# Optimization experiments

Measured on AMD Instinct MI355X. Metric: run time of the kernel, lower is better.

## Reference

```python
import jax, jax.numpy as jnp
import numpy as np

N_TARGETS = 4
BATCH_SIZE = 4
B = N_TARGETS * BATCH_SIZE
N_SAMPLES = 1024
LAYERS = [(128, 128), (256, 64), (512, 32)]  # (channels, spatial)
EPS_COS = 1e-10


def setup_inputs() -> dict:
    key = jax.random.key(0)
    inp = {}
    for l, (c, s) in enumerate(LAYERS):
        k1, k2, k3, k4, key = jax.random.split(key, 5)
        n = s * s
        inp[f't{l}'] = jax.random.normal(k1, (N_TARGETS, c, s, s), dtype=jnp.float32)
        inp[f'g{l}'] = jax.random.normal(k2, (B, c, s, s), dtype=jnp.float32)
        inp[f'ix{l}'] = jax.random.randint(k3, (B, N_SAMPLES), 0, n)
        inp[f'iy{l}'] = jax.random.randint(k4, (B, N_SAMPLES), 0, n)
    return inp


def _cos_remd(x, y):
    # x: (b,n,c), y: (b,m,c)
    xn = jnp.linalg.norm(x, axis=2, keepdims=True)            # (b,n,1)
    yn = jnp.linalg.norm(y, axis=2, keepdims=True)            # (b,m,1)
    cross = jnp.einsum('bnc,bmc->bnm', x, y)                  # (b,n,m)
    dist = 1.0 - cross / (xn * yn.transpose(0, 2, 1) + EPS_COS)
    m1 = dist.min(axis=1).mean(axis=1)                        # min over n, mean over m
    m2 = dist.min(axis=2).mean(axis=1)                        # min over m, mean over n
    return jnp.maximum(m1, m2)                                # (b,)


def _moment_loss(x, y):
    mu_x = x.mean(axis=1, keepdims=True)
    mu_y = y.mean(axis=1, keepdims=True)
    mu_diff = jnp.abs(mu_x - mu_y).mean(axis=(1, 2))
    x_c = x - mu_x
    y_c = y - mu_y
    x_cov = jnp.einsum('bnc,bnd->bcd', x_c, x_c) / (x.shape[1] - 1)
    y_cov = jnp.einsum('bmc,bmd->bcd', y_c, y_c) / (y.shape[1] - 1)
    cov_diff = jnp.abs(x_cov - y_cov).mean(axis=(1, 2))
    return mu_diff + cov_diff                                 # (b,)


def _layer_loss(t, g, ix, iy):
    b, c, h, w = g.shape
    y = jnp.tile(t, (BATCH_SIZE, 1, 1, 1)).reshape(b, t.shape[1], -1)  # (b,c,n_y)
    x = g.reshape(b, c, -1)                                            # (b,c,n_x)
    x = jnp.take_along_axis(x, ix[:, None, :], axis=2)                 # (b,c,ns)
    y = jnp.take_along_axis(y, iy[:, None, :], axis=2)                 # (b,c,ns)
    x = x.transpose(0, 2, 1)
    y = y.transpose(0, 2, 1)
    return _cos_remd(x, y) + _moment_loss(x, y)


def reference(t0, g0, t1, g1, t2, g2, ix0, iy0, ix1, iy1, ix2, iy2):
    loss = (_layer_loss(t0, g0, ix0, iy0)
            + _layer_loss(t1, g1, ix1, iy1)
            + _layer_loss(t2, g2, ix2, iy2))
    return loss.reshape(BATCH_SIZE, N_TARGETS).mean(axis=0)   # (n_targets,)
```

## Files before the change

kernel.cpp:

```cpp
#include <hip/hip_runtime.h>
#include <math.h>

#define NT 4
#define BSZ 4
#define BB 16
#define NS 1024
#define CHF 1024
#define NBUF 4
#define MAXL 3

typedef unsigned short u16;
typedef __attribute__((ext_vector_type(8))) short bf16x8;
typedef __attribute__((ext_vector_type(4))) float f32x4;

struct LayerP {
    const float *g, *t;
    const int *ix, *iy;
    u16 *Xt, *Yt, *Xs, *Ys;
    float *xp, *yp;
    float *rxn, *ryn;
    float *sx, *sy;
    unsigned *m1u, *m2u;
    float *cov;
    int C, n, nchunk, ntri, lid;
};
struct Tab {
    LayerP L[MAXL];
    int nl, nb, b0, ysh;
    float* losspart;
};

__device__ __forceinline__ unsigned fenc(float f) {
    unsigned u = __float_as_uint(f);
    return (u & 0x80000000u) ? ~u : (u | 0x80000000u);
}
__device__ __forceinline__ float fdec(unsigned u) {
    unsigned v = (u & 0x80000000u) ? (u & 0x7FFFFFFFu) : ~u;
    return __uint_as_float(v);
}
__device__ __forceinline__ u16 f2bf(float f) {
    unsigned u = __float_as_uint(f);
    unsigned r = u + 0x7FFFu + ((u >> 16) & 1u);
    return (u16)(r >> 16);
}
__device__ __forceinline__ float bf2f(u16 h) {
    return __uint_as_float((unsigned)h << 16);
}

__device__ __forceinline__ void gload16(const float* src, float* dst) {
    __builtin_amdgcn_global_load_lds(
        (const __attribute__((address_space(1))) float*)src,
        (__attribute__((address_space(3))) float*)dst, 16, 0, 0);
}
__device__ __forceinline__ void wait_rem(int rem) {
    if (rem >= 2)      asm volatile("s_waitcnt vmcnt(2)" ::: "memory");
    else if (rem == 1) asm volatile("s_waitcnt vmcnt(1)" ::: "memory");
    else               asm volatile("s_waitcnt vmcnt(0)" ::: "memory");
}

__global__ __launch_bounds__(256) void gather_x(Tab tab)
{
    int x = blockIdx.x, l = 0;
    while (l < MAXL - 1 && x >= tab.L[l].C) { x -= tab.L[l].C; ++l; }
    const LayerP P = tab.L[l];
    int c = x, bl = blockIdx.y, bg = tab.b0 + bl;
    int tid = threadIdx.x;
    int wv = tid >> 6, lane = tid & 63;
    const float* __restrict__ grow = P.g + ((size_t)bg * P.C + c) * P.n;
    const int* __restrict__ ixr = P.ix + bg * NS;
    __shared__ __align__(16) float buf[NBUF][CHF];
    __shared__ float red[4];
    int px[4];
    float xv[4] = {0.f, 0.f, 0.f, 0.f};
    #pragma unroll
    for (int r = 0; r < 4; ++r) px[r] = ixr[tid + r * 256];
    int nch = P.n >> 10;
    int npro = nch < 3 ? nch : 3;
    for (int d = 0; d < npro; ++d)
        gload16(grow + d * CHF + wv * 256 + lane * 4, &buf[d][wv * 256]);
    for (int ch = 0; ch < nch; ++ch) {
        int rem = nch - 1 - ch; if (rem > 2) rem = 2;
        wait_rem(rem);
        __builtin_amdgcn_s_barrier();
        __builtin_amdgcn_sched_barrier(0);
        if (ch + 3 < nch)
            gload16(grow + (ch + 3) * CHF + wv * 256 + lane * 4, &buf[(ch + 3) & 3][wv * 256]);
        int lo = ch * CHF;
        #pragma unroll
        for (int r = 0; r < 4; ++r) {
            int rel = px[r] - lo;
            if ((unsigned)rel < (unsigned)CHF) xv[r] = buf[ch & 3][rel];
        }
    }
    u16* __restrict__ xo = P.Xt + ((size_t)bl * P.C + c) * NS;
    float ax = 0.f;
    #pragma unroll
    for (int r = 0; r < 4; ++r) {
        u16 hb = f2bf(xv[r]);
        xo[tid + r * 256] = hb;
        ax += bf2f(hb);
    }
    for (int o = 32; o > 0; o >>= 1) ax += __shfl_down(ax, o);
    if (lane == 0) red[wv] = ax;
    __syncthreads();
    if (tid == 0) P.sx[bl * P.C + c] = red[0] + red[1] + red[2] + red[3];
}

__global__ __launch_bounds__(256) void gather_y(Tab tab)
{
    int x = blockIdx.x, l = 0;
    while (l < MAXL - 1 && x >= tab.L[l].C) { x -= tab.L[l].C; ++l; }
    const LayerP P = tab.L[l];
    int c = x, grp = blockIdx.y;
    int tid = threadIdx.x;
    int wv = tid >> 6, lane = tid & 63;
    int nk, tgt, bls[4];
    if (tab.ysh == NT) {
        nk = 4; tgt = grp;
        #pragma unroll
        for (int k = 0; k < 4; ++k) bls[k] = grp + NT * k;
    } else {
        nk = 1; bls[0] = grp; tgt = (tab.b0 + grp) % NT;
        bls[1] = bls[2] = bls[3] = 0;
    }
    const float* __restrict__ trow = P.t + ((size_t)tgt * P.C + c) * P.n;
    __shared__ __align__(16) float buf[NBUF][CHF];
    __shared__ float red[4][4];
    int py[4][4];
    float yv[4][4];
    #pragma unroll
    for (int k = 0; k < 4; ++k) {
        if (k < nk) {
            const int* iyr = P.iy + (tab.b0 + bls[k]) * NS;
            #pragma unroll
            for (int r = 0; r < 4; ++r) { py[k][r] = iyr[tid + r * 256]; yv[k][r] = 0.f; }
        }
    }
    int nch = P.n >> 10;
    int npro = nch < 3 ? nch : 3;
    for (int d = 0; d < npro; ++d)
        gload16(trow + d * CHF + wv * 256 + lane * 4, &buf[d][wv * 256]);
    for (int ch = 0; ch < nch; ++ch) {
        int rem = nch - 1 - ch; if (rem > 2) rem = 2;
        wait_rem(rem);
        __builtin_amdgcn_s_barrier();
        __builtin_amdgcn_sched_barrier(0);
        if (ch + 3 < nch)
            gload16(trow + (ch + 3) * CHF + wv * 256 + lane * 4, &buf[(ch + 3) & 3][wv * 256]);
        int lo = ch * CHF;
        #pragma unroll
        for (int k = 0; k < 4; ++k)
            if (k < nk) {
                #pragma unroll
                for (int r = 0; r < 4; ++r) {
                    int rel = py[k][r] - lo;
                    if ((unsigned)rel < (unsigned)CHF) yv[k][r] = buf[ch & 3][rel];
                }
            }
    }
    #pragma unroll
    for (int k = 0; k < 4; ++k) {
        if (k >= nk) break;
        u16* __restrict__ yo = P.Yt + ((size_t)bls[k] * P.C + c) * NS;
        float ay = 0.f;
        #pragma unroll
        for (int r = 0; r < 4; ++r) {
            u16 hb = f2bf(yv[k][r]);
            yo[tid + r * 256] = hb;
            ay += bf2f(hb);
        }
        for (int o = 32; o > 0; o >>= 1) ay += __shfl_down(ay, o);
        if (lane == 0) red[k][wv] = ay;
    }
    __syncthreads();
    if (tid < nk)
        P.sy[bls[tid] * P.C + c] = red[tid][0] + red[tid][1] + red[tid][2] + red[tid][3];
}

__global__ void transpose_k(Tab tab)
{
    int x = blockIdx.x, l = 0;
    while (l < MAXL - 1 && x >= tab.L[l].C / 64) { x -= tab.L[l].C / 64; ++l; }
    const LayerP P = tab.L[l];
    int z = blockIdx.z;
    int bl = z >> 1, which = z & 1;
    const u16* __restrict__ Zt = which ? P.Yt : P.Xt;
    u16* __restrict__ Zs = which ? P.Ys : P.Xs;
    float* __restrict__ zp = which ? P.yp : P.xp;
    int C = P.C;
    int ctile = x;
    int c0 = ctile * 64, s0 = blockIdx.y * 64;
    __shared__ __align__(16) u16 T[64][72];
    int tid = threadIdx.x;
    #pragma unroll
    for (int rep = 0; rep < 2; ++rep) {
        int q = tid + rep * 256;
        int rr = q >> 3, seg = q & 7;
        *(float4*)&T[rr][seg * 8] =
            *(const float4*)&Zt[((size_t)bl * C + c0 + rr) * NS + s0 + seg * 8];
    }
    __syncthreads();
    #pragma unroll
    for (int rep = 0; rep < 2; ++rep) {
        int q = tid + rep * 256;
        int sr = q >> 3, cs = q & 7;
        __align__(16) u16 tmp[8];
        float p = 0.f;
        #pragma unroll
        for (int e = 0; e < 8; ++e) {
            u16 h = T[cs * 8 + e][sr];
            tmp[e] = h;
            float v = bf2f(h);
            p = fmaf(v, v, p);
        }
        *(float4*)&Zs[((size_t)bl * NS + s0 + sr) * C + c0 + cs * 8] = *(float4*)tmp;
        p += __shfl_xor(p, 1);
        p += __shfl_xor(p, 2);
        p += __shfl_xor(p, 4);
        if (cs == 0)
            zp[((size_t)bl * P.nchunk + ctile) * NS + s0 + sr] = p;
    }
}

__global__ void colnorm_reduce(Tab tab)
{
    const LayerP P = tab.L[blockIdx.y];
    int bl = blockIdx.z;
    int s = blockIdx.x * 256 + threadIdx.x;
    float ax = 0.f, ay = 0.f;
    for (int k = 0; k < P.nchunk; ++k) {
        size_t o = ((size_t)bl * P.nchunk + k) * NS + s;
        ax += P.xp[o];
        ay += P.yp[o];
    }
    P.rxn[bl * NS + s] = rsqrtf(ax);
    P.ryn[bl * NS + s] = rsqrtf(ay);
    P.m1u[bl * NS + s] = 0xFFFFFFFFu;
    P.m2u[bl * NS + s] = 0xFFFFFFFFu;
}

__global__ __launch_bounds__(256) void cross_mfma(Tab tab)
{
    int z = blockIdx.z;
    int l = z / tab.nb, bl = z - l * tab.nb;
    const LayerP P = tab.L[l];
    int C = P.C;
    int i0 = blockIdx.x * 128, j0 = blockIdx.y * 128;
    __shared__ __align__(16) u16 As[128][40], Bs[128][40];
    int tid = threadIdx.x;
    int w = tid >> 6, lane = tid & 63;
    int wr = w >> 1, wc = w & 1;
    int q = lane >> 4, r = lane & 15;
    const u16* __restrict__ Xb = P.Xs + ((size_t)bl * NS + i0) * C;
    const u16* __restrict__ Yb = P.Ys + ((size_t)bl * NS + j0) * C;
    f32x4 acc[4][4];
    #pragma unroll
    for (int m = 0; m < 4; ++m)
        #pragma unroll
        for (int nn = 0; nn < 4; ++nn) acc[m][nn] = (f32x4){0.f, 0.f, 0.f, 0.f};

    for (int kk = 0; kk < C; kk += 32) {
        __syncthreads();
        #pragma unroll
        for (int rep = 0; rep < 2; ++rep) {
            int qid = tid + rep * 256;
            int row = qid >> 2, seg = qid & 3;
            size_t off = (size_t)row * C + kk + seg * 8;
            *(float4*)&As[row][seg * 8] = *(const float4*)&Xb[off];
            *(float4*)&Bs[row][seg * 8] = *(const float4*)&Yb[off];
        }
        __syncthreads();
        bf16x8 a[4], b[4];
        #pragma unroll
        for (int m = 0; m < 4; ++m)
            a[m] = *(const bf16x8*)&As[wr * 64 + m * 16 + r][q * 8];
        #pragma unroll
        for (int nn = 0; nn < 4; ++nn)
            b[nn] = *(const bf16x8*)&Bs[wc * 64 + nn * 16 + r][q * 8];
        #pragma unroll
        for (int m = 0; m < 4; ++m)
            #pragma unroll
            for (int nn = 0; nn < 4; ++nn)
                acc[m][nn] = __builtin_amdgcn_mfma_f32_16x16x32_bf16(a[m], b[nn], acc[m][nn], 0, 0, 0);
    }

    float rxl[4][4], ryl[4];
    #pragma unroll
    for (int m = 0; m < 4; ++m)
        #pragma unroll
        for (int reg = 0; reg < 4; ++reg)
            rxl[m][reg] = P.rxn[bl * NS + i0 + wr * 64 + m * 16 + q * 4 + reg];
    #pragma unroll
    for (int nn = 0; nn < 4; ++nn)
        ryl[nn] = P.ryn[bl * NS + j0 + wc * 64 + nn * 16 + r];

    float rm[4][4], cm[4];
    #pragma unroll
    for (int m = 0; m < 4; ++m)
        #pragma unroll
        for (int reg = 0; reg < 4; ++reg) rm[m][reg] = 1e30f;
    #pragma unroll
    for (int nn = 0; nn < 4; ++nn) cm[nn] = 1e30f;
    #pragma unroll
    for (int m = 0; m < 4; ++m)
        #pragma unroll
        for (int nn = 0; nn < 4; ++nn)
            #pragma unroll
            for (int reg = 0; reg < 4; ++reg) {
                float d = 1.f - acc[m][nn][reg] * rxl[m][reg] * ryl[nn];
                rm[m][reg] = fminf(rm[m][reg], d);
                cm[nn] = fminf(cm[nn], d);
            }
    #pragma unroll
    for (int m = 0; m < 4; ++m)
        #pragma unroll
        for (int reg = 0; reg < 4; ++reg) {
            float v = rm[m][reg];
            v = fminf(v, __shfl_xor(v, 1));
            v = fminf(v, __shfl_xor(v, 2));
            v = fminf(v, __shfl_xor(v, 4));
            v = fminf(v, __shfl_xor(v, 8));
            rm[m][reg] = v;
        }
    if (r == 0) {
        #pragma unroll
        for (int m = 0; m < 4; ++m)
            #pragma unroll
            for (int reg = 0; reg < 4; ++reg) {
                int i = i0 + wr * 64 + m * 16 + q * 4 + reg;
                atomicMin(&P.m2u[bl * NS + i], fenc(rm[m][reg]));
            }
    }
    #pragma unroll
    for (int nn = 0; nn < 4; ++nn) {
        float v = cm[nn];
        v = fminf(v, __shfl_xor(v, 16));
        v = fminf(v, __shfl_xor(v, 32));
        cm[nn] = v;
    }
    if (q == 0) {
        #pragma unroll
        for (int nn = 0; nn < 4; ++nn) {
            int j = j0 + wc * 64 + nn * 16 + r;
            atomicMin(&P.m1u[bl * NS + j], fenc(cm[nn]));
        }
    }
}

__global__ __launch_bounds__(256) void cov_mfma(Tab tab)
{
    int x = blockIdx.x, l = 0;
    while (l < MAXL - 1 && x >= tab.L[l].ntri) { x -= tab.L[l].ntri; ++l; }
    const LayerP P = tab.L[l];
    int u = x;
    int bl = blockIdx.y;
    int C = P.C;
    int ty = 0;
    while ((ty + 1) * (ty + 2) / 2 <= u) ++ty;
    int tx = u - ty * (ty + 1) / 2;
    int c0 = ty * 128, d0 = tx * 128;
    float wgt = (tx == ty) ? 1.f : 2.f;

    __shared__ __align__(16) u16 As[128][40], Bs[128][40], Cs2[128][40], Ds[128][40];
    int tid = threadIdx.x;
    int w = tid >> 6, lane = tid & 63;
    int wr = w >> 1, wc = w & 1;
    int q = lane >> 4, r = lane & 15;
    const u16* __restrict__ Xc = P.Xt + ((size_t)bl * C + c0) * NS;
    const u16* __restrict__ Xd = P.Xt + ((size_t)bl * C + d0) * NS;
    const u16* __restrict__ Yc = P.Yt + ((size_t)bl * C + c0) * NS;
    const u16* __restrict__ Yd = P.Yt + ((size_t)bl * C + d0) * NS;

    f32x4 accX[4][4], accY[4][4];
    #pragma unroll
    for (int m = 0; m < 4; ++m)
        #pragma unroll
        for (int nn = 0; nn < 4; ++nn) {
            accX[m][nn] = (f32x4){0.f, 0.f, 0.f, 0.f};
            accY[m][nn] = (f32x4){0.f, 0.f, 0.f, 0.f};
        }

    for (int ss = 0; ss < NS; ss += 32) {
        __syncthreads();
        #pragma unroll
        for (int rep = 0; rep < 2; ++rep) {
            int qid = tid + rep * 256;
            int row = qid >> 2, seg = qid & 3;
            size_t off = (size_t)row * NS + ss + seg * 8;
            *(float4*)&As[row][seg * 8]  = *(const float4*)&Xc[off];
            *(float4*)&Bs[row][seg * 8]  = *(const float4*)&Xd[off];
            *(float4*)&Cs2[row][seg * 8] = *(const float4*)&Yc[off];
            *(float4*)&Ds[row][seg * 8]  = *(const float4*)&Yd[off];
        }
        __syncthreads();
        {
            bf16x8 a[4], b[4];
            #pragma unroll
            for (int m = 0; m < 4; ++m) a[m] = *(const bf16x8*)&As[wr * 64 + m * 16 + r][q * 8];
            #pragma unroll
            for (int nn = 0; nn < 4; ++nn) b[nn] = *(const bf16x8*)&Bs[wc * 64 + nn * 16 + r][q * 8];
            #pragma unroll
            for (int m = 0; m < 4; ++m)
                #pragma unroll
                for (int nn = 0; nn < 4; ++nn)
                    accX[m][nn] = __builtin_amdgcn_mfma_f32_16x16x32_bf16(a[m], b[nn], accX[m][nn], 0, 0, 0);
        }
        {
            bf16x8 a[4], b[4];
            #pragma unroll
            for (int m = 0; m < 4; ++m) a[m] = *(const bf16x8*)&Cs2[wr * 64 + m * 16 + r][q * 8];
            #pragma unroll
            for (int nn = 0; nn < 4; ++nn) b[nn] = *(const bf16x8*)&Ds[wc * 64 + nn * 16 + r][q * 8];
            #pragma unroll
            for (int m = 0; m < 4; ++m)
                #pragma unroll
                for (int nn = 0; nn < 4; ++nn)
                    accY[m][nn] = __builtin_amdgcn_mfma_f32_16x16x32_bf16(a[m], b[nn], accY[m][nn], 0, 0, 0);
        }
    }

    float scxv[4][4], scyv[4][4], sdxv[4], sdyv[4];
    #pragma unroll
    for (int m = 0; m < 4; ++m)
        #pragma unroll
        for (int reg = 0; reg < 4; ++reg) {
            int c = c0 + wr * 64 + m * 16 + q * 4 + reg;
            scxv[m][reg] = P.sx[bl * C + c];
            scyv[m][reg] = P.sy[bl * C + c];
        }
    #pragma unroll
    for (int nn = 0; nn < 4; ++nn) {
        int d = d0 + wc * 64 + nn * 16 + r;
        sdxv[nn] = P.sx[bl * C + d];
        sdyv[nn] = P.sy[bl * C + d];
    }
    const float invNS = 1.f / NS, invNSm1 = 1.f / (NS - 1);
    float tsum = 0.f;
    #pragma unroll
    for (int m = 0; m < 4; ++m)
        #pragma unroll
        for (int nn = 0; nn < 4; ++nn)
            #pragma unroll
            for (int reg = 0; reg < 4; ++reg) {
                float cx = (accX[m][nn][reg] - scxv[m][reg] * sdxv[nn] * invNS) * invNSm1;
                float cy = (accY[m][nn][reg] - scyv[m][reg] * sdyv[nn] * invNS) * invNSm1;
                tsum += fabsf(cx - cy);
            }
    tsum *= wgt;
    __shared__ float redc[4];
    for (int o = 32; o > 0; o >>= 1) tsum += __shfl_down(tsum, o);
    if (lane == 0) redc[w] = tsum;
    __syncthreads();
    if (tid == 0)
        P.cov[(size_t)bl * P.ntri + u] = redc[0] + redc[1] + redc[2] + redc[3];
}

__global__ void finalize_kernel(Tab tab)
{
    const LayerP P = tab.L[blockIdx.x];
    int bl = blockIdx.y;
    int tid = threadIdx.x;
    int C = P.C;
    float s1 = 0.f, s2 = 0.f, smu = 0.f, scov = 0.f;
    for (int s = tid; s < NS; s += 256) {
        s1 += fdec(P.m1u[bl * NS + s]);
        s2 += fdec(P.m2u[bl * NS + s]);
    }
    for (int c = tid; c < C; c += 256) smu += fabsf(P.sx[bl * C + c] - P.sy[bl * C + c]);
    for (int i = tid; i < P.ntri; i += 256) scov += P.cov[(size_t)bl * P.ntri + i];
    __shared__ float red[4][4];
    for (int o = 32; o > 0; o >>= 1) {
        s1 += __shfl_down(s1, o);
        s2 += __shfl_down(s2, o);
        smu += __shfl_down(smu, o);
        scov += __shfl_down(scov, o);
    }
    int wid = tid >> 6, lane = tid & 63;
    if (lane == 0) { red[0][wid] = s1; red[1][wid] = s2; red[2][wid] = smu; red[3][wid] = scov; }
    __syncthreads();
    if (tid == 0) {
        s1 = red[0][0] + red[0][1] + red[0][2] + red[0][3];
        s2 = red[1][0] + red[1][1] + red[1][2] + red[1][3];
        smu = red[2][0] + red[2][1] + red[2][2] + red[2][3];
        scov = red[3][0] + red[3][1] + red[3][2] + red[3][3];
        float m1m = s1 * (1.f / NS), m2m = s2 * (1.f / NS);
        float mu_diff = smu * (1.f / NS) * (1.f / (float)C);
        float cov_diff = scov / ((float)C * (float)C);
        tab.losspart[(tab.b0 + bl) * 3 + P.lid] = fmaxf(m1m, m2m) + mu_diff + cov_diff;
    }
}

__global__ void out_kernel(const float* __restrict__ lp, float* __restrict__ out)
{
    int t = threadIdx.x;
    if (t < NT) {
        float s = 0.f;
        for (int k = 0; k < BSZ; ++k)
            for (int l = 0; l < 3; ++l)
                s += lp[(k * NT + t) * 3 + l];
        out[t] = s * (1.f / BSZ);
    }
}

static inline size_t alignup(size_t v) { return (v + 255) & ~(size_t)255; }

static size_t layer_bytes(int C, int nb) {
    int nchunk = C / 64;
    int tc = C / 128, ntri = tc * (tc + 1) / 2;
    size_t szZ = alignup((size_t)NS * C * 2);
    size_t szP = alignup((size_t)nchunk * NS * 4);
    return (size_t)nb * (4 * szZ + 2 * szP + 4 * alignup(NS * 4)
                         + 2 * alignup(C * 4) + alignup(ntri * 4));
}

static char* fill_layer(LayerP& P, char* p, int C, int n, int nb, int lid,
                        const float* g, const float* t, const int* ix, const int* iy) {
    P.g = g; P.t = t; P.ix = ix; P.iy = iy;
    P.C = C; P.n = n; P.lid = lid;
    P.nchunk = C / 64;
    int tc = C / 128;
    P.ntri = tc * (tc + 1) / 2;
    size_t szZ = alignup((size_t)NS * C * 2);
    size_t szP = alignup((size_t)P.nchunk * NS * 4);
    P.Xt = (u16*)p;  p += nb * szZ;
    P.Yt = (u16*)p;  p += nb * szZ;
    P.Xs = (u16*)p;  p += nb * szZ;
    P.Ys = (u16*)p;  p += nb * szZ;
    P.xp = (float*)p; p += nb * szP;
    P.yp = (float*)p; p += nb * szP;
    P.rxn = (float*)p; p += nb * alignup(NS * 4);
    P.ryn = (float*)p; p += nb * alignup(NS * 4);
    P.m1u = (unsigned*)p; p += nb * alignup(NS * 4);
    P.m2u = (unsigned*)p; p += nb * alignup(NS * 4);
    P.sx = (float*)p; p += nb * alignup(C * 4);
    P.sy = (float*)p; p += nb * alignup(C * 4);
    P.cov = (float*)p; p += nb * alignup(P.ntri * 4);
    return p;
}

static void launch_group(const Tab& tab, hipStream_t stream) {
    int sumC = 0, sumC64 = 0, sumNtri = 0;
    for (int l = 0; l < tab.nl; ++l) {
        sumC += tab.L[l].C;
        sumC64 += tab.L[l].C / 64;
        sumNtri += tab.L[l].ntri;
    }
    int nb = tab.nb;
    int ygrid = (tab.ysh == NT) ? NT : nb;
    gather_x<<<dim3(sumC, nb), 256, 0, stream>>>(tab);
    gather_y<<<dim3(sumC, ygrid), 256, 0, stream>>>(tab);
    transpose_k<<<dim3(sumC64, NS / 64, nb * 2), 256, 0, stream>>>(tab);
    colnorm_reduce<<<dim3(NS / 256, tab.nl, nb), 256, 0, stream>>>(tab);
    cross_mfma<<<dim3(NS / 128, NS / 128, tab.nl * nb), 256, 0, stream>>>(tab);
    cov_mfma<<<dim3(sumNtri, nb), 256, 0, stream>>>(tab);
    finalize_kernel<<<dim3(tab.nl, nb), 256, 0, stream>>>(tab);
}

extern "C" void kernel_launch(void* const* d_in, const int* in_sizes, int n_in,
                              void* d_out, int out_size, void* d_ws, size_t ws_size,
                              hipStream_t stream)
{
    const float* tp[3] = {(const float*)d_in[0], (const float*)d_in[4], (const float*)d_in[8]};
    const float* gp[3] = {(const float*)d_in[1], (const float*)d_in[5], (const float*)d_in[9]};
    const int* ixp[3]  = {(const int*)d_in[2], (const int*)d_in[6], (const int*)d_in[10]};
    const int* iyp[3]  = {(const int*)d_in[3], (const int*)d_in[7], (const int*)d_in[11]};
    const int Cs[3] = {128, 256, 512};
    const int Sp[3] = {128, 64, 32};

    float* out = (float*)d_out;
    char* ws = (char*)d_ws;
    float* losspart = (float*)ws;
    size_t base = alignup(BB * 3 * 4);
    size_t avail = (ws_size > base) ? ws_size - base : 0;

    size_t need_all = 0;
    for (int l = 0; l < 3; ++l) need_all += layer_bytes(Cs[l], BB);

    if (avail >= need_all) {
        Tab tab;
        tab.nl = 3; tab.nb = BB; tab.b0 = 0; tab.ysh = NT; tab.losspart = losspart;
        char* p = ws + base;
        for (int l = 0; l < 3; ++l)
            p = fill_layer(tab.L[l], p, Cs[l], Sp[l] * Sp[l], BB, l,
                           gp[l], tp[l], ixp[l], iyp[l]);
        launch_group(tab, stream);
    } else {
        for (int l = 0; l < 3; ++l) {
            size_t per_b = layer_bytes(Cs[l], 1);
            int G = (int)(avail / per_b);
            if (G > BB) G = BB;
            if (G < 1) G = 1;
            for (int b0 = 0; b0 < BB; b0 += G) {
                int nb = (BB - b0 < G) ? (BB - b0) : G;
                Tab tab;
                tab.nl = 1; tab.nb = nb; tab.b0 = b0; tab.ysh = 1; tab.losspart = losspart;
                fill_layer(tab.L[0], ws + base, Cs[l], Sp[l] * Sp[l], nb, l,
                           gp[l], tp[l], ixp[l], iyp[l]);
                launch_group(tab, stream);
            }
        }
    }
    out_kernel<<<1, 64, 0, stream>>>(losspart, out);
}
```

Measured before the change: 238.3 us.

## Merge gather kernels and split large spatial rows across blocks

Fuses gather_x and gather_y into one flat-grid gather kernel and splits each spatial row into slices of up to four 1024-float chunks, so layer 0 (16 chunks) is handled by four blocks instead of one serial block. Each block issues all of its chunk loads into LDS up front instead of running a rolling three-deep prefetch. Per-slice partial channel sums go to new psx/psy buffers, which colnorm_reduce then adds into sx/sy. This is meant to cut the serial streaming latency of the large layer and one kernel launch, at the cost of extra partial-sum traffic and more blocks that each reload the index arrays.

Measured after the change: 228.1 us. 4.3% less time.

```diff
diff --git a/kernel.cpp b/kernel.cpp
--- a/kernel.cpp
+++ b/kernel.cpp
@@ -6,7 +6,6 @@
 #define BB 16
 #define NS 1024
 #define CHF 1024
-#define NBUF 4
 #define MAXL 3
 
 typedef unsigned short u16;
@@ -18,11 +17,12 @@
     const int *ix, *iy;
     u16 *Xt, *Yt, *Xs, *Ys;
     float *xp, *yp;
+    float *psx, *psy;
     float *rxn, *ryn;
     float *sx, *sy;
     unsigned *m1u, *m2u;
     float *cov;
-    int C, n, nchunk, ntri, lid;
+    int C, n, nchunk, ntri, lid, hs, csl, xblk, yblk;
 };
 struct Tab {
     LayerP L[MAXL];
@@ -53,128 +53,137 @@
         (__attribute__((address_space(3))) float*)dst, 16, 0, 0);
 }
 __device__ __forceinline__ void wait_rem(int rem) {
-    if (rem >= 2)      asm volatile("s_waitcnt vmcnt(2)" ::: "memory");
+    if (rem >= 3)      asm volatile("s_waitcnt vmcnt(3)" ::: "memory");
+    else if (rem == 2) asm volatile("s_waitcnt vmcnt(2)" ::: "memory");
     else if (rem == 1) asm volatile("s_waitcnt vmcnt(1)" ::: "memory");
     else               asm volatile("s_waitcnt vmcnt(0)" ::: "memory");
 }
 
-__global__ __launch_bounds__(256) void gather_x(Tab tab)
-{
-    int x = blockIdx.x, l = 0;
-    while (l < MAXL - 1 && x >= tab.L[l].C) { x -= tab.L[l].C; ++l; }
+__global__ __launch_bounds__(256) void gather(Tab tab)
+{
+    int f = blockIdx.x;
+    int l = 0, side = 0, c = 0, grp = 0, h = 0;
+    #pragma unroll
+    for (int li = 0; li < MAXL; ++li) {
+        if (li >= tab.nl) break;
+        if (f < tab.L[li].xblk) { l = li; side = 0; goto decoded; }
+        f -= tab.L[li].xblk;
+        if (f < tab.L[li].yblk) { l = li; side = 1; goto decoded; }
+        f -= tab.L[li].yblk;
+    }
+decoded:;
     const LayerP P = tab.L[l];
-    int c = x, bl = blockIdx.y, bg = tab.b0 + bl;
+    c = f % P.C; f /= P.C;
+    int ytg = (tab.ysh == NT) ? NT : tab.nb;
+    int gdim = side ? ytg : tab.nb;
+    grp = f % gdim; h = f / gdim;
+
     int tid = threadIdx.x;
     int wv = tid >> 6, lane = tid & 63;
-    const float* __restrict__ grow = P.g + ((size_t)bg * P.C + c) * P.n;
-    const int* __restrict__ ixr = P.ix + bg * NS;
-    __shared__ __align__(16) float buf[NBUF][CHF];
-    __shared__ float red[4];
-    int px[4];
-    float xv[4] = {0.f, 0.f, 0.f, 0.f};
-    #pragma unroll
-    for (int r = 0; r < 4; ++r) px[r] = ixr[tid + r * 256];
-    int nch = P.n >> 10;
-    int npro = nch < 3 ? nch : 3;
-    for (int d = 0; d < npro; ++d)
-        gload16(grow + d * CHF + wv * 256 + lane * 4, &buf[d][wv * 256]);
-    for (int ch = 0; ch < nch; ++ch) {
-        int rem = nch - 1 - ch; if (rem > 2) rem = 2;
-        wait_rem(rem);
-        __builtin_amdgcn_s_barrier();
+    int csl = P.csl;
+    int sbase = h * csl * CHF;
+    __shared__ __align__(16) float buf[4][CHF];
+    __shared__ float red[4][4];
+
+    if (side == 0) {
+        int bl = grp, bg = tab.b0 + bl;
+        const float* __restrict__ grow = P.g + ((size_t)bg * P.C + c) * P.n;
+        const int* __restrict__ ixr = P.ix + bg * NS;
+        int px[4];
+        #pragma unroll
+        for (int r = 0; r < 4; ++r) px[r] = ixr[tid + r * 256] - sbase;
         __builtin_amdgcn_sched_barrier(0);
-        if (ch + 3 < nch)
-            gload16(grow + (ch + 3) * CHF + wv * 256 + lane * 4, &buf[(ch + 3) & 3][wv * 256]);
-        int lo = ch * CHF;
+        for (int d = 0; d < csl; ++d)
+            gload16(grow + sbase + d * CHF + wv * 256 + lane * 4, &buf[d][wv * 256]);
+        float xv[4] = {0.f, 0.f, 0.f, 0.f};
+        for (int ch = 0; ch < csl; ++ch) {
+            wait_rem(csl - 1 - ch);
+            __builtin_amdgcn_s_barrier();
+            __builtin_amdgcn_sched_barrier(0);
+            #pragma unroll
+            for (int r = 0; r < 4; ++r) {
+                int rel = px[r] - ch * CHF;
+                if ((unsigned)rel < (unsigned)CHF) xv[r] = buf[ch][rel];
+            }
+        }
+        u16* __restrict__ xo = P.Xt + ((size_t)bl * P.C + c) * NS;
+        float ax = 0.f;
         #pragma unroll
         for (int r = 0; r < 4; ++r) {
-            int rel = px[r] - lo;
-            if ((unsigned)rel < (unsigned)CHF) xv[r] = buf[ch & 3][rel];
-        }
-    }
-    u16* __restrict__ xo = P.Xt + ((size_t)bl * P.C + c) * NS;
-    float ax = 0.f;
-    #pragma unroll
-    for (int r = 0; r < 4; ++r) {
-        u16 hb = f2bf(xv[r]);
-        xo[tid + r * 256] = hb;
-        ax += bf2f(hb);
-    }
-    for (int o = 32; o > 0; o >>= 1) ax += __shfl_down(ax, o);
-    if (lane == 0) red[wv] = ax;
-    __syncthreads();
-    if (tid == 0) P.sx[bl * P.C + c] = red[0] + red[1] + red[2] + red[3];
-}
-
-__global__ __launch_bounds__(256) void gather_y(Tab tab)
-{
-    int x = blockIdx.x, l = 0;
-    while (l < MAXL - 1 && x >= tab.L[l].C) { x -= tab.L[l].C; ++l; }
-    const LayerP P = tab.L[l];
-    int c = x, grp = blockIdx.y;
-    int tid = threadIdx.x;
-    int wv = tid >> 6, lane = tid & 63;
-    int nk, tgt, bls[4];
-    if (tab.ysh == NT) {
-        nk = 4; tgt = grp;
-        #pragma unroll
-        for (int k = 0; k < 4; ++k) bls[k] = grp + NT * k;
+            if ((unsigned)px[r] < (unsigned)(csl * CHF)) {
+                u16 hb = f2bf(xv[r]);
+                xo[tid + r * 256] = hb;
+                ax += bf2f(hb);
+            }
+        }
+        for (int o = 32; o > 0; o >>= 1) ax += __shfl_down(ax, o);
+        if (lane == 0) red[0][wv] = ax;
+        __syncthreads();
+        if (tid == 0)
+            P.psx[((size_t)h * tab.nb + bl) * P.C + c] =
+                red[0][0] + red[0][1] + red[0][2] + red[0][3];
     } else {
-        nk = 1; bls[0] = grp; tgt = (tab.b0 + grp) % NT;
-        bls[1] = bls[2] = bls[3] = 0;
-    }
-    const float* __restrict__ trow = P.t + ((size_t)tgt * P.C + c) * P.n;
-    __shared__ __align__(16) float buf[NBUF][CHF];
-    __shared__ float red[4][4];
-    int py[4][4];
-    float yv[4][4];
-    #pragma unroll
-    for (int k = 0; k < 4; ++k) {
-        if (k < nk) {
-            const int* iyr = P.iy + (tab.b0 + bls[k]) * NS;
-            #pragma unroll
-            for (int r = 0; r < 4; ++r) { py[k][r] = iyr[tid + r * 256]; yv[k][r] = 0.f; }
-        }
-    }
-    int nch = P.n >> 10;
-    int npro = nch < 3 ? nch : 3;
-    for (int d = 0; d < npro; ++d)
-        gload16(trow + d * CHF + wv * 256 + lane * 4, &buf[d][wv * 256]);
-    for (int ch = 0; ch < nch; ++ch) {
-        int rem = nch - 1 - ch; if (rem > 2) rem = 2;
-        wait_rem(rem);
-        __builtin_amdgcn_s_barrier();
-        __builtin_amdgcn_sched_barrier(0);
-        if (ch + 3 < nch)
-            gload16(trow + (ch + 3) * CHF + wv * 256 + lane * 4, &buf[(ch + 3) & 3][wv * 256]);
-        int lo = ch * CHF;
+        int nk, tgt, bls[4];
+        if (tab.ysh == NT) {
+            nk = 4; tgt = grp;
+            #pragma unroll
+            for (int k = 0; k < 4; ++k) bls[k] = tgt + NT * k;
+        } else {
+            nk = 1; bls[0] = grp; tgt = (tab.b0 + grp) % NT;
+            bls[1] = bls[2] = bls[3] = 0;
+        }
+        const float* __restrict__ trow = P.t + ((size_t)tgt * P.C + c) * P.n;
+        int py[4][4];
         #pragma unroll
         for (int k = 0; k < 4; ++k)
             if (k < nk) {
+                const int* iyr = P.iy + (tab.b0 + bls[k]) * NS;
                 #pragma unroll
-                for (int r = 0; r < 4; ++r) {
-                    int rel = py[k][r] - lo;
-                    if ((unsigned)rel < (unsigned)CHF) yv[k][r] = buf[ch & 3][rel];
+                for (int r = 0; r < 4; ++r) py[k][r] = iyr[tid + r * 256] - sbase;
+            }
+        __builtin_amdgcn_sched_barrier(0);
+        for (int d = 0; d < csl; ++d)
+            gload16(trow + sbase + d * CHF + wv * 256 + lane * 4, &buf[d][wv * 256]);
+        float yv[4][4];
+        #pragma unroll
+        for (int k = 0; k < 4; ++k)
+            #pragma unroll
+            for (int r = 0; r < 4; ++r) yv[k][r] = 0.f;
+        for (int ch = 0; ch < csl; ++ch) {
+            wait_rem(csl - 1 - ch);
+            __builtin_amdgcn_s_barrier();
+            __builtin_amdgcn_sched_barrier(0);
+            #pragma unroll
+            for (int k = 0; k < 4; ++k)
+                if (k < nk) {
+                    #pragma unroll
+                    for (int r = 0; r < 4; ++r) {
+                        int rel = py[k][r] - ch * CHF;
+                        if ((unsigned)rel < (unsigned)CHF) yv[k][r] = buf[ch][rel];
+                    }
                 }
-            }
-    }
-    #pragma unroll
-    for (int k = 0; k < 4; ++k) {
-        if (k >= nk) break;
-        u16* __restrict__ yo = P.Yt + ((size_t)bls[k] * P.C + c) * NS;
-        float ay = 0.f;
-        #pragma unroll
-        for (int r = 0; r < 4; ++r) {
-            u16 hb = f2bf(yv[k][r]);
-            yo[tid + r * 256] = hb;
-            ay += bf2f(hb);
-        }
-        for (int o = 32; o > 0; o >>= 1) ay += __shfl_down(ay, o);
-        if (lane == 0) red[k][wv] = ay;
-    }
-    __syncthreads();
-    if (tid < nk)
-        P.sy[bls[tid] * P.C + c] = red[tid][0] + red[tid][1] + red[tid][2] + red[tid][3];
+        }
+        #pragma unroll
+        for (int k = 0; k < 4; ++k) {
+            if (k >= nk) break;
+            u16* __restrict__ yo = P.Yt + ((size_t)bls[k] * P.C + c) * NS;
+            float ay = 0.f;
+            #pragma unroll
+            for (int r = 0; r < 4; ++r) {
+                if ((unsigned)py[k][r] < (unsigned)(csl * CHF)) {
+                    u16 hb = f2bf(yv[k][r]);
+                    yo[tid + r * 256] = hb;
+                    ay += bf2f(hb);
+                }
+            }
+            for (int o = 32; o > 0; o >>= 1) ay += __shfl_down(ay, o);
+            if (lane == 0) red[k][wv] = ay;
+        }
+        __syncthreads();
+        if (tid < nk)
+            P.psy[((size_t)h * tab.nb + bls[tid]) * P.C + c] =
+                red[tid][0] + red[tid][1] + red[tid][2] + red[tid][3];
+    }
 }
 
 __global__ void transpose_k(Tab tab)
@@ -226,6 +235,7 @@
 {
     const LayerP P = tab.L[blockIdx.y];
     int bl = blockIdx.z;
+    int nb = tab.nb;
     int s = blockIdx.x * 256 + threadIdx.x;
     float ax = 0.f, ay = 0.f;
     for (int k = 0; k < P.nchunk; ++k) {
@@ -237,6 +247,16 @@
     P.ryn[bl * NS + s] = rsqrtf(ay);
     P.m1u[bl * NS + s] = 0xFFFFFFFFu;
     P.m2u[bl * NS + s] = 0xFFFFFFFFu;
+    int cq = P.C >> 2;
+    for (int c = blockIdx.x * cq + threadIdx.x; c < (blockIdx.x + 1) * cq; c += 256) {
+        float sx = 0.f, sy = 0.f;
+        for (int h = 0; h < P.hs; ++h) {
+            sx += P.psx[((size_t)h * nb + bl) * P.C + c];
+            sy += P.psy[((size_t)h * nb + bl) * P.C + c];
+        }
+        P.sx[bl * P.C + c] = sx;
+        P.sy[bl * P.C + c] = sy;
+    }
 }
 
 __global__ __launch_bounds__(256) void cross_mfma(Tab tab)
@@ -504,30 +524,46 @@
 
 static inline size_t alignup(size_t v) { return (v + 255) & ~(size_t)255; }
 
-static size_t layer_bytes(int C, int nb) {
+static void geo(int n, int& hs, int& csl) {
+    int nch = n >> 10;
+    if (nch < 1) nch = 1;
+    hs = (nch >= 4) ? nch / 4 : 1;
+    csl = nch / hs;
+}
+
+static size_t layer_bytes(int C, int n, int nb) {
     int nchunk = C / 64;
     int tc = C / 128, ntri = tc * (tc + 1) / 2;
+    int hs, csl; geo(n, hs, csl);
     size_t szZ = alignup((size_t)NS * C * 2);
     size_t szP = alignup((size_t)nchunk * NS * 4);
+    size_t szPS = alignup((size_t)hs * nb * C * 4);
     return (size_t)nb * (4 * szZ + 2 * szP + 4 * alignup(NS * 4)
-                         + 2 * alignup(C * 4) + alignup(ntri * 4));
-}
-
-static char* fill_layer(LayerP& P, char* p, int C, int n, int nb, int lid,
+                         + 2 * alignup(C * 4) + alignup(ntri * 4))
+           + 2 * szPS;
+}
+
+static char* fill_layer(LayerP& P, char* p, int C, int n, int nb, int ysh, int lid,
                         const float* g, const float* t, const int* ix, const int* iy) {
     P.g = g; P.t = t; P.ix = ix; P.iy = iy;
     P.C = C; P.n = n; P.lid = lid;
     P.nchunk = C / 64;
     int tc = C / 128;
     P.ntri = tc * (tc + 1) / 2;
+    geo(n, P.hs, P.csl);
+    P.xblk = C * P.hs * nb;
+    P.yblk = C * P.hs * ((ysh == NT) ? NT : nb);
     size_t szZ = alignup((size_t)NS * C * 2);
     size_t szP = alignup((size_t)P.nchunk * NS * 4);
+    size_t szPS = alignup((size_t)P.hs * nb * C * 4);
     P.Xt = (u16*)p;  p += nb * szZ;
     P.Yt = (u16*)p;  p += nb * szZ;
     P.Xs = (u16*)p;  p += nb * szZ;
     P.Ys = (u16*)p;  p += nb * szZ;
     P.xp = (float*)p; p += nb * szP;
     P.yp = (float*)p; p += nb * szP;
+    P.psx = (float*)p; p += szPS;
+    P.psy = (float*)p; p += szPS;
     P.rxn = (float*)p; p += nb * alignup(NS * 4);
     P.ryn = (float*)p; p += nb * alignup(NS * 4);
     P.m1u = (unsigned*)p; p += nb * alignup(NS * 4);
@@ -539,16 +575,14 @@
 }
 
 static void launch_group(const Tab& tab, hipStream_t stream) {
-    int sumC = 0, sumC64 = 0, sumNtri = 0;
+    int sumC64 = 0, sumNtri = 0, flatN = 0;
     for (int l = 0; l < tab.nl; ++l) {
-        sumC += tab.L[l].C;
         sumC64 += tab.L[l].C / 64;
         sumNtri += tab.L[l].ntri;
+        flatN += tab.L[l].xblk + tab.L[l].yblk;
     }
     int nb = tab.nb;
-    int ygrid = (tab.ysh == NT) ? NT : nb;
-    gather_x<<<dim3(sumC, nb), 256, 0, stream>>>(tab);
-    gather_y<<<dim3(sumC, ygrid), 256, 0, stream>>>(tab);
+    gather<<<flatN, 256, 0, stream>>>(tab);
     transpose_k<<<dim3(sumC64, NS / 64, nb * 2), 256, 0, stream>>>(tab);
     colnorm_reduce<<<dim3(NS / 256, tab.nl, nb), 256, 0, stream>>>(tab);
     cross_mfma<<<dim3(NS / 128, NS / 128, tab.nl * nb), 256, 0, stream>>>(tab);
@@ -574,19 +608,19 @@
     size_t avail = (ws_size > base) ? ws_size - base : 0;
 
     size_t need_all = 0;
-    for (int l = 0; l < 3; ++l) need_all += layer_bytes(Cs[l], BB);
+    for (int l = 0; l < 3; ++l) need_all += layer_bytes(Cs[l], Sp[l] * Sp[l], BB);
 
     if (avail >= need_all) {
         Tab tab;
         tab.nl = 3; tab.nb = BB; tab.b0 = 0; tab.ysh = NT; tab.losspart = losspart;
         char* p = ws + base;
         for (int l = 0; l < 3; ++l)
-            p = fill_layer(tab.L[l], p, Cs[l], Sp[l] * Sp[l], BB, l,
+            p = fill_layer(tab.L[l], p, Cs[l], Sp[l] * Sp[l], BB, NT, l,
                            gp[l], tp[l], ixp[l], iyp[l]);
         launch_group(tab, stream);
     } else {
         for (int l = 0; l < 3; ++l) {
-            size_t per_b = layer_bytes(Cs[l], 1);
+            size_t per_b = layer_bytes(Cs[l], Sp[l] * Sp[l], 1);
             int G = (int)(avail / per_b);
             if (G > BB) G = BB;
             if (G < 1) G = 1;
@@ -594,7 +628,7 @@
                 int nb = (BB - b0 < G) ? (BB - b0) : G;
                 Tab tab;
                 tab.nl = 1; tab.nb = nb; tab.b0 = b0; tab.ysh = 1; tab.losspart = losspart;
-                fill_layer(tab.L[0], ws + base, Cs[l], Sp[l] * Sp[l], nb, l,
+                fill_layer(tab.L[0], ws + base, Cs[l], Sp[l] * Sp[l], nb, 1, l,
                            gp[l], tp[l], ixp[l], iyp[l]);
                 launch_group(tab, stream);
             }
```
